# Optimization experiments

Measured on AMD Instinct MI355X. Metric: run time of the kernel, lower is better.

## Reference

```python
import jax, jax.numpy as jnp
import numpy as np

HID = 2048
NH = 16
HD = HID // NH  # 128
EPS = 1e-6
BASE = 10000.0


def _rmsnorm(x, w):
    xf = x.astype(jnp.float32)
    y = xf * jax.lax.rsqrt(jnp.mean(xf * xf, axis=-1, keepdims=True) + EPS)
    return y.astype(x.dtype) * w


def _rope_cos_sin(seq_len, dtype):
    inv_freq = 1.0 / (BASE ** (jnp.arange(0, HD, 2, dtype=jnp.float32) / HD))
    t = jnp.arange(seq_len, dtype=jnp.float32)
    freqs = jnp.outer(t, inv_freq)          # [S, HD/2]
    emb = jnp.concatenate([freqs, freqs], axis=-1)  # [S, HD]
    return jnp.cos(emb).astype(dtype), jnp.sin(emb).astype(dtype)


def _rotate_half(x):
    x1, x2 = jnp.split(x, 2, axis=-1)
    return jnp.concatenate([-x2, x1], axis=-1)


def setup_inputs() -> dict:
    key = jax.random.key(0)
    ks = jax.random.split(key, 8)
    B, S = 2, 2048
    s = 0.02
    return {
        "hidden_states": jax.random.normal(ks[0], (B, S, HID), jnp.float32),
        "Wq": jax.random.normal(ks[1], (HID, HID), jnp.float32) * s,
        "Wk": jax.random.normal(ks[2], (HID, HID), jnp.float32) * s,
        "Wv": jax.random.normal(ks[3], (HID, HID), jnp.float32) * s,
        "Wo": jax.random.normal(ks[4], (HID, HID), jnp.float32) * s,
        "w1": jax.random.normal(ks[5], (HID, HID), jnp.float32) * s,
        "w2": jax.random.normal(ks[6], (HID, HID), jnp.float32) * s,
        "w3": jax.random.normal(ks[7], (HID, HID), jnp.float32) * s,
        "ln1_w": jnp.ones((HID,), jnp.float32),
        "ln2_w": jnp.ones((HID,), jnp.float32),
    }


def reference(hidden_states, Wq, Wk, Wv, Wo, w1, w2, w3, ln1_w, ln2_w):
    B, S, _ = hidden_states.shape
    residual = hidden_states
    x = _rmsnorm(hidden_states, ln1_w)

    # projections -> [B, NH, S, HD]
    q = (x @ Wq).reshape(B, S, NH, HD).transpose(0, 2, 1, 3)
    k = (x @ Wk).reshape(B, S, NH, HD).transpose(0, 2, 1, 3)
    v = (x @ Wv).reshape(B, S, NH, HD).transpose(0, 2, 1, 3)

    cos, sin = _rope_cos_sin(S, x.dtype)  # [S, HD]
    cos = cos[None, None]  # broadcast over batch and heads
    sin = sin[None, None]
    q = q * cos + _rotate_half(q) * sin
    k = k * cos + _rotate_half(k) * sin

    scores = jnp.einsum("bhqd,bhkd->bhqk", q, k) / np.sqrt(HD).astype(np.float32)
    # no attention_mask (torch default path). fp32 softmax.
    attn = jax.nn.softmax(scores.astype(jnp.float32), axis=-1).astype(q.dtype)
    ctx = jnp.einsum("bhqk,bhkd->bhqd", attn, v)  # [B, NH, S, HD]
    ctx = ctx.transpose(0, 2, 1, 3).reshape(B, S, HID)
    attn_out = ctx @ Wo

    h = residual + attn_out
    residual = h
    y = _rmsnorm(h, ln2_w)
    mlp = (jax.nn.silu(y @ w1) * (y @ w3)) @ w2
    return residual + mlp
```

## Files before the change

### kernel.cpp

```cpp
#include <hip/hip_runtime.h>

#define HIDN 2048
#define NHEAD 16
#define HD 128
#define SEQ 2048
#define BATCH 2
#define NROWS (BATCH*SEQ)

typedef __bf16 bf16_t;
typedef bf16_t bf16x8 __attribute__((ext_vector_type(8)));
typedef float f32x4 __attribute__((ext_vector_type(4)));

#define AS1 __attribute__((address_space(1)))
#define AS3 __attribute__((address_space(3)))

__device__ __forceinline__ unsigned short f2bf(float x) {
  union { bf16_t b; unsigned short u; } cv; cv.b = (bf16_t)x; return cv.u;
}

#define MFMA16(a,b,c) __builtin_amdgcn_mfma_f32_16x16x32_bf16((a),(b),(c),0,0,0)

__device__ __forceinline__ void gload16(const void* g, void* l) {
  __builtin_amdgcn_global_load_lds((const AS1 void*)g, (AS3 void*)l, 16, 0, 0);
}

__global__ __launch_bounds__(256) void transpose_all_kernel(
    const float* __restrict__ Wq, const float* __restrict__ Wk,
    const float* __restrict__ Wv, const float* __restrict__ Wo,
    const float* __restrict__ w1, const float* __restrict__ w3,
    const float* __restrict__ w2, unsigned short* __restrict__ wblk) {
  const int z = blockIdx.z;
  const float* W; unsigned short* dstb; int tmode = 0, half = 0;
  switch (z) {
    case 0: W = Wq; dstb = wblk;                       tmode = 1; break;
    case 1: W = Wk; dstb = wblk + (size_t)2048 * HIDN; tmode = 1; break;
    case 2: W = Wv; dstb = wblk + (size_t)4096 * HIDN; break;
    case 3: W = Wo; dstb = wblk + (size_t)6144 * HIDN; break;
    case 4: W = w1; dstb = wblk + (size_t)8192 * HIDN; tmode = 2; half = 0; break;
    case 5: W = w3; dstb = wblk + (size_t)8192 * HIDN; tmode = 2; half = 1; break;
    default: W = w2; dstb = wblk + (size_t)12288 * HIDN; break;
  }
  __shared__ float t[64][69];
  const int tid = threadIdx.x;
  const int bn = blockIdx.x * 64, bk = blockIdx.y * 64;
  const int lc = (tid & 15) * 4, lrw = tid >> 4;
#pragma unroll
  for (int i = 0; i < 4; ++i) {
    int k = bk + lrw + i * 16;
    float4 v = *(const float4*)(W + (long)k * HIDN + bn + lc);
    t[lrw + i * 16][lc] = v.x; t[lrw + i * 16][lc + 1] = v.y;
    t[lrw + i * 16][lc + 2] = v.z; t[lrw + i * 16][lc + 3] = v.w;
  }
  __syncthreads();
  const int nl = tid >> 2, k0 = (tid & 3) * 16;
  int n = bn + nl;
  int dst;
  if (tmode == 0) dst = n;
  else if (tmode == 1) { int d = n & 127; dst = (n & ~127) | ((d & 63) << 1) | (d >> 6); }
  else dst = (n >> 4) * 32 + half * 16 + (n & 15);
  unsigned short* orow = dstb + (long)dst * HIDN + bk + k0;
#pragma unroll
  for (int j = 0; j < 16; j += 4) {
    ushort4 o;
    o.x = f2bf(t[k0 + j][nl]);     o.y = f2bf(t[k0 + j + 1][nl]);
    o.z = f2bf(t[k0 + j + 2][nl]); o.w = f2bf(t[k0 + j + 3][nl]);
    *(ushort4*)(orow + j) = o;
  }
}

__global__ void rope_table_kernel(float* __restrict__ cosT, float* __restrict__ sinT) {
  int s = blockIdx.x, d = threadIdx.x;
  float invf = powf(10000.0f, (-2.0f * (float)d) / 128.0f);
  float ang = (float)s * invf;
  cosT[s * 64 + d] = cosf(ang);
  sinT[s * 64 + d] = sinf(ang);
}

__global__ __launch_bounds__(256) void rmsnorm_kernel(
    const float* __restrict__ x, const float* __restrict__ w, unsigned short* __restrict__ out) {
  long row = blockIdx.x;
  const float* xr = x + row * HIDN;
  int c0 = threadIdx.x * 4;
  float4 v0 = *(const float4*)(xr + c0);
  float4 v1 = *(const float4*)(xr + 1024 + c0);
  float s = v0.x*v0.x + v0.y*v0.y + v0.z*v0.z + v0.w*v0.w
          + v1.x*v1.x + v1.y*v1.y + v1.z*v1.z + v1.w*v1.w;
#pragma unroll
  for (int off = 1; off < 64; off <<= 1) s += __shfl_xor(s, off);
  __shared__ float red[4];
  if ((threadIdx.x & 63) == 0) red[threadIdx.x >> 6] = s;
  __syncthreads();
  float tot = red[0] + red[1] + red[2] + red[3];
  float r = 1.0f / sqrtf(tot * (1.0f / (float)HIDN) + 1e-6f);
  float4 w0 = *(const float4*)(w + c0);
  float4 w1 = *(const float4*)(w + 1024 + c0);
  ushort4 o0, o1;
  o0.x = f2bf(v0.x * r * w0.x); o0.y = f2bf(v0.y * r * w0.y);
  o0.z = f2bf(v0.z * r * w0.z); o0.w = f2bf(v0.w * r * w0.w);
  o1.x = f2bf(v1.x * r * w1.x); o1.y = f2bf(v1.y * r * w1.y);
  o1.z = f2bf(v1.z * r * w1.z); o1.w = f2bf(v1.w * r * w1.w);
  *(ushort4*)(out + row * HIDN + c0) = o0;
  *(ushort4*)(out + row * HIDN + 1024 + c0) = o1;
}

template <int MODE>
__global__ __launch_bounds__(512, 2) void gemm256_kernel(
    const unsigned short* __restrict__ A, const unsigned short* __restrict__ Bt,
    int nbx,
    void* __restrict__ p0, void* __restrict__ p1, void* __restrict__ p2,
    const float* __restrict__ cosT, const float* __restrict__ sinT) {
  __shared__ unsigned short L[65536];
  const int tid = threadIdx.x;
  const int wave = tid >> 6, lane = tid & 63;
  const int lr = lane & 15, lkg = lane >> 4;
  const int wr = wave >> 2, wc = wave & 3;
  const int nwg = (int)gridDim.x;
  const int bid = (int)blockIdx.x;
  const int wg = (bid & 7) * (nwg >> 3) + (bid >> 3);
  const int bx = wg % nbx, by = wg / nbx;
  const long bm = (long)by * 256, bn = (long)bx * 256;
  const int srow = wave * 8 + (lane >> 3);
  const int sslot = (lane & 7) ^ (lane >> 3);
  const unsigned short* Ag = A + (bm + srow) * HIDN + sslot * 8;
  const unsigned short* Bg = Bt + (bn + srow) * HIDN + sslot * 8;
  f32x4 acc[8][4] = {};

#define STAGE256(kt2)                                                            \
  {                                                                              \
    const long ko = (long)(kt2) * 64;                                            \
    unsigned short* Ld = &L[((kt2) & 1) * 32768];                                \
    _Pragma("unroll")                                                            \
    for (int j = 0; j < 4; ++j) {                                                \
      gload16(Ag + ko + (long)j * 64 * HIDN, &Ld[(j * 64 + wave * 8) * 64]);     \
      gload16(Bg + ko + (long)j * 64 * HIDN, &Ld[16384 + (j * 64 + wave * 8) * 64]); \
    }                                                                            \
  }

  STAGE256(0);
  STAGE256(1);
  asm volatile("s_waitcnt vmcnt(8)" ::: "memory");
  __builtin_amdgcn_sched_barrier(0);
  __builtin_amdgcn_s_barrier();

  for (int kt = 0; kt < 32; ++kt) {
    const int d = kt & 1;
    const char* Lb = (const char*)L + d * 65536;
    bf16x8 bfr[4][2];
#pragma unroll
    for (int n = 0; n < 4; ++n) {
      int row = wc * 64 + n * 16 + lr;
      int x7 = row & 7;
#pragma unroll
      for (int ks = 0; ks < 2; ++ks) {
        int s = ks * 4 + lkg;
        bfr[n][ks] = *(const bf16x8*)(Lb + 32768 + row * 128 + ((s ^ x7) << 4));
      }
    }
#pragma unroll
    for (int q = 0; q < 4; ++q) {
      bf16x8 af[2][2];
#pragma unroll
      for (int mm = 0; mm < 2; ++mm) {
        int row = wr * 128 + (q * 2 + mm) * 16 + lr;
        int x7 = row & 7;
#pragma unroll
        for (int ks = 0; ks < 2; ++ks) {
          int s = ks * 4 + lkg;
          af[mm][ks] = *(const bf16x8*)(Lb + row * 128 + ((s ^ x7) << 4));
        }
      }
      __builtin_amdgcn_s_setprio(1);
#pragma unroll
      for (int mm = 0; mm < 2; ++mm)
#pragma unroll
        for (int n = 0; n < 4; ++n) {
          acc[q * 2 + mm][n] = MFMA16(af[mm][0], bfr[n][0], acc[q * 2 + mm][n]);
          acc[q * 2 + mm][n] = MFMA16(af[mm][1], bfr[n][1], acc[q * 2 + mm][n]);
        }
      __builtin_amdgcn_s_setprio(0);
    }
    if (kt == 31) break;
    asm volatile("s_waitcnt lgkmcnt(0)" ::: "memory");
    __builtin_amdgcn_sched_barrier(0);
    __builtin_amdgcn_s_barrier();
    if (kt < 30) {
      STAGE256(kt + 2);
      asm volatile("s_waitcnt vmcnt(8)" ::: "memory");
    } else {
      asm volatile("s_waitcnt vmcnt(0)" ::: "memory");
    }
    __builtin_amdgcn_sched_barrier(0);
    __builtin_amdgcn_s_barrier();
  }
#undef STAGE256

  const int gc0 = (int)bn + wc * 64;
  if (MODE == 1) {
    unsigned short* bout = (unsigned short*)p0;
#pragma unroll
    for (int m = 0; m < 8; ++m) {
      long r0 = bm + wr * 128 + m * 16 + lkg * 4;
#pragma unroll
      for (int n = 0; n < 4; n += 2) {
        int ggrp = (gc0 + n * 16) >> 5;
        long c = (long)ggrp * 16 + lr;
#pragma unroll
        for (int r = 0; r < 4; ++r) {
          float x = acc[m][n][r], g = acc[m][n + 1][r];
          float sv = x / (1.0f + __expf(-x)) * g;
          bout[(r0 + r) * 2048 + c] = f2bf(sv);
        }
      }
    }
  } else {
    int bufid = gc0 >> 11;
    if (bufid == 2) {
      unsigned short* vT = (unsigned short*)p2;
#pragma unroll
      for (int m = 0; m < 8; ++m) {
        long r0 = bm + wr * 128 + m * 16 + lkg * 4;
        long bq = r0 >> 11;
        int s = (int)(r0 & 2047);
#pragma unroll
        for (int n = 0; n < 4; ++n) {
          int wcol = (gc0 + n * 16 + lr) & 2047;
          int hh = wcol >> 7, dd = wcol & 127;
          ushort4 pw;
          pw.x = f2bf(acc[m][n][0]); pw.y = f2bf(acc[m][n][1]);
          pw.z = f2bf(acc[m][n][2]); pw.w = f2bf(acc[m][n][3]);
          *(ushort4*)(vT + ((bq * 16 + hh) * 128 + dd) * (long)SEQ + s) = pw;
        }
      }
    } else {
      unsigned short* dst = (bufid == 0) ? (unsigned short*)p0 : (unsigned short*)p1;
      const float qscale = (bufid == 0) ? 0.08838834764831845f : 1.0f;
#pragma unroll
      for (int m = 0; m < 8; ++m) {
        long r0 = bm + wr * 128 + m * 16 + lkg * 4;
#pragma unroll
        for (int n = 0; n < 4; ++n) {
          int wcol = (gc0 + n * 16 + lr) & 2047;
          int f = wcol & 127, hh = wcol >> 7;
          int j = f >> 1, odd = f & 1;
          int oc = hh * 128 + (odd ? 64 : 0) + j;
#pragma unroll
          for (int r = 0; r < 4; ++r) {
            long row = r0 + r;
            int s = (int)(row & (SEQ - 1));
            float cv = cosT[s * 64 + j], sn = sinT[s * 64 + j];
            float v = acc[m][n][r];
            float o = __shfl_xor(v, 1);
            float res = (odd ? (v * cv + o * sn) : (v * cv - o * sn)) * qscale;
            dst[row * 2048 + oc] = f2bf(res);
          }
        }
      }
    }
  }
}

template <int MODE>
__global__ __launch_bounds__(256) void gemm_kernel(
    const unsigned short* __restrict__ A, const unsigned short* __restrict__ Bt, int N,
    void* __restrict__ p0, const void* __restrict__ p1) {
  __shared__ unsigned short As[128 * 32];
  __shared__ unsigned short Bs[128 * 32];
  const int tid = threadIdx.x;
  const int lane = tid & 63, wave = tid >> 6;
  const int wm = (wave >> 1) * 64, wn = (wave & 1) * 64;
  const int lr = lane & 15, lkg = lane >> 4;
  const long bm = (long)blockIdx.y * 128, bn = (long)blockIdx.x * 128;
  f32x4 acc[4][4] = {};
  const int rA0 = wave * 32 + (lane >> 2);
  const int gs0 = (lane & 3) ^ ((rA0 >> 1) & 3);
  const int gs1 = (lane & 3) ^ (((rA0 + 16) >> 1) & 3);
  const unsigned short* Ag0 = A + (bm + rA0) * HIDN + gs0 * 8;
  const unsigned short* Ag1 = A + (bm + rA0 + 16) * HIDN + gs1 * 8;
  const unsigned short* Bg0 = Bt + (bn + rA0) * HIDN + gs0 * 8;
  const unsigned short* Bg1 = Bt + (bn + rA0 + 16) * HIDN + gs1 * 8;
  unsigned short* lA0 = &As[(wave * 32) * 32];
  unsigned short* lA1 = &As[(wave * 32 + 16) * 32];
  unsigned short* lB0 = &Bs[(wave * 32) * 32];
  unsigned short* lB1 = &Bs[(wave * 32 + 16) * 32];
  for (int k0 = 0; k0 < HIDN; k0 += 32) {
    __syncthreads();
    gload16(Ag0 + k0, lA0);
    gload16(Ag1 + k0, lA1);
    gload16(Bg0 + k0, lB0);
    gload16(Bg1 + k0, lB1);
    __syncthreads();
    bf16x8 af[4], bfr[4];
#pragma unroll
    for (int m = 0; m < 4; ++m) {
      int row = wm + m * 16 + lr;
      af[m] = *(const bf16x8*)((const char*)As + row * 64 + ((lkg ^ ((row >> 1) & 3)) << 4));
    }
#pragma unroll
    for (int n = 0; n < 4; ++n) {
      int row = wn + n * 16 + lr;
      bfr[n] = *(const bf16x8*)((const char*)Bs + row * 64 + ((lkg ^ ((row >> 1) & 3)) << 4));
    }
#pragma unroll
    for (int m = 0; m < 4; ++m)
#pragma unroll
      for (int n = 0; n < 4; ++n) acc[m][n] = MFMA16(af[m], bfr[n], acc[m][n]);
  }
  float* fout = (float*)p0;
  const float* addsrc = (const float*)p1;
#pragma unroll
  for (int m = 0; m < 4; ++m)
#pragma unroll
    for (int n = 0; n < 4; ++n) {
      long r0 = bm + wm + m * 16 + lkg * 4;
      long c = bn + wn + n * 16 + lr;
#pragma unroll
      for (int r = 0; r < 4; ++r) {
        long idx = (r0 + r) * 2048 + c;
        if (MODE == 2) fout[idx] = addsrc[idx] + acc[m][n][r];
        else fout[idx] = fout[idx] + acc[m][n][r];
      }
    }
}

__global__ __launch_bounds__(256) void flash_attn_kernel(
    const unsigned short* __restrict__ Q, const unsigned short* __restrict__ Kb,
    const unsigned short* __restrict__ vT, unsigned short* __restrict__ O) {
  __shared__ unsigned short Ks[2][64 * 128];
  __shared__ unsigned short Vs[2][128 * 64];
  __shared__ unsigned short Ps[4][16][72];
  const int qt = blockIdx.x, h = blockIdx.y, b = blockIdx.z;
  const int tid = threadIdx.x, wave = tid >> 6, lane = tid & 63;
  const int lr = lane & 15, lkg = lane >> 4, lk = lkg * 8;
  const long rowbase = (long)b * SEQ;
  const int qrow0 = qt * 64 + wave * 16;
  bf16x8 aq[4];
#pragma unroll
  for (int ks = 0; ks < 4; ++ks)
    aq[ks] = *(const bf16x8*)(Q + (rowbase + qrow0 + lr) * HIDN + h * HD + ks * 32 + lk);
  const unsigned short* vbase = vT + ((long)(b * 16 + h) * 128) * SEQ;
  const int krl = lane >> 4;
  const int vrl = lane >> 3, vch = lane & 7;
  f32x4 acc[8] = {};
  float m_ = -3.0e38f, l_ = 0.f;

#define STAGEKV(t_, kv0_)                                                          \
  {                                                                                \
    _Pragma("unroll")                                                              \
    for (int j = 0; j < 4; ++j) {                                                  \
      int rl = wave * 16 + j * 4 + krl;                                            \
      int slot = (lane & 15) ^ (rl & 15);                                          \
      gload16(Kb + (rowbase + (kv0_) + rl) * HIDN + h * HD + slot * 8,             \
              &Ks[(t_) & 1][(wave * 16 + j * 4) * 128]);                           \
    }                                                                              \
    _Pragma("unroll")                                                              \
    for (int j = 0; j < 4; ++j) {                                                  \
      int dd = wave * 32 + j * 8 + vrl;                                            \
      int slot = vch ^ (dd & 7);                                                   \
      gload16(vbase + (long)dd * SEQ + (kv0_) + slot * 8,                          \
              &Vs[(t_) & 1][(wave * 32 + j * 8) * 64]);                            \
    }                                                                              \
  }

  STAGEKV(0, 0);

  for (int t = 0; t < SEQ / 64; ++t) {
    asm volatile("s_waitcnt vmcnt(0)" ::: "memory");
    asm volatile("s_barrier" ::: "memory");
    if (t + 1 < SEQ / 64) STAGEKV(t + 1, (long)(t + 1) * 64);
    const char* ksb = (const char*)Ks[t & 1];
    f32x4 sa[4] = {};
#pragma unroll
    for (int n = 0; n < 4; ++n) {
      int row = n * 16 + lr;
#pragma unroll
      for (int ks = 0; ks < 4; ++ks) {
        bf16x8 bk = *(const bf16x8*)(ksb + row * 256 + (((ks * 4 + lkg) ^ (row & 15)) << 4));
        sa[n] = MFMA16(bk, aq[ks], sa[n]);
      }
    }
    float pmax = sa[0][0];
#pragma unroll
    for (int n = 0; n < 4; ++n)
#pragma unroll
      for (int r = 0; r < 4; ++r) pmax = fmaxf(pmax, sa[n][r]);
    pmax = fmaxf(pmax, __shfl_xor(pmax, 16));
    pmax = fmaxf(pmax, __shfl_xor(pmax, 32));
    if (__all(pmax - m_ <= 8.0f)) {
      float psum = 0.f;
#pragma unroll
      for (int n = 0; n < 4; ++n)
#pragma unroll
        for (int r = 0; r < 4; ++r) {
          float p = __expf(sa[n][r] - m_);
          sa[n][r] = p;
          psum += p;
        }
      psum += __shfl_xor(psum, 16);
      psum += __shfl_xor(psum, 32);
      l_ += psum;
    } else {
      float mnew = fmaxf(m_, pmax);
      float corr = __expf(m_ - mnew);
      float psum = 0.f;
#pragma unroll
      for (int n = 0; n < 4; ++n)
#pragma unroll
        for (int r = 0; r < 4; ++r) {
          float p = __expf(sa[n][r] - mnew);
          sa[n][r] = p;
          psum += p;
        }
      psum += __shfl_xor(psum, 16);
      psum += __shfl_xor(psum, 32);
      l_ = l_ * corr + psum;
      m_ = mnew;
      float corr4[4];
#pragma unroll
      for (int r = 0; r < 4; ++r) corr4[r] = __shfl(corr, 4 * lkg + r);
#pragma unroll
      for (int df = 0; df < 8; ++df)
#pragma unroll
        for (int r = 0; r < 4; ++r) acc[df][r] *= corr4[r];
    }
#pragma unroll
    for (int n = 0; n < 4; ++n) {
      ushort4 pw;
      pw.x = f2bf(sa[n][0]); pw.y = f2bf(sa[n][1]);
      pw.z = f2bf(sa[n][2]); pw.w = f2bf(sa[n][3]);
      *(ushort4*)&Ps[wave][lr][n * 16 + 4 * lkg] = pw;
    }
    bf16x8 pa0 = *(const bf16x8*)&Ps[wave][lr][lk];
    bf16x8 pa1 = *(const bf16x8*)&Ps[wave][lr][32 + lk];
    const char* vsb = (const char*)Vs[t & 1];
#pragma unroll
    for (int df = 0; df < 8; ++df) {
      int row = df * 16 + lr;
      int x7 = row & 7;
      bf16x8 bv0 = *(const bf16x8*)(vsb + row * 128 + ((lkg ^ x7) << 4));
      bf16x8 bv1 = *(const bf16x8*)(vsb + row * 128 + (((4 + lkg) ^ x7) << 4));
      acc[df] = MFMA16(pa0, bv0, acc[df]);
      acc[df] = MFMA16(pa1, bv1, acc[df]);
    }
    asm volatile("s_barrier" ::: "memory");
  }
#undef STAGEKV
  float invl = 1.0f / l_;
  float invl4[4];
#pragma unroll
  for (int r = 0; r < 4; ++r) invl4[r] = __shfl(invl, 4 * lkg + r);
#pragma unroll
  for (int r = 0; r < 4; ++r) {
    long orow = rowbase + qrow0 + lkg * 4 + r;
#pragma unroll
    for (int df = 0; df < 8; ++df)
      O[orow * HIDN + h * HD + df * 16 + lr] = f2bf(acc[df][r] * invl4[r]);
  }
}

extern "C" void kernel_launch(void* const* d_in, const int* in_sizes, int n_in,
                              void* d_out, int out_size, void* d_ws, size_t ws_size,
                              hipStream_t stream) {
  const float* hidden = (const float*)d_in[0];
  const float* Wq = (const float*)d_in[1];
  const float* Wk = (const float*)d_in[2];
  const float* Wv = (const float*)d_in[3];
  const float* Wo = (const float*)d_in[4];
  const float* w1 = (const float*)d_in[5];
  const float* w2 = (const float*)d_in[6];
  const float* w3 = (const float*)d_in[7];
  const float* ln1 = (const float*)d_in[8];
  const float* ln2 = (const float*)d_in[9];
  float* out = (float*)d_out;

  char* ws = (char*)d_ws;
  size_t off = 0;
  auto alloc = [&](size_t bytes) -> void* {
    void* p = ws + off;
    off += (bytes + 255) & ~(size_t)255;
    return p;
  };
  unsigned short* wblk = (unsigned short*)alloc((size_t)(2048L * 6 + 2048) * HIDN * 2);
  unsigned short* wQ = wblk;
  unsigned short* wG = wblk + (size_t)8192 * HIDN;
  unsigned short* wO = wblk + (size_t)6144 * HIDN;
  unsigned short* wD = wblk + (size_t)12288 * HIDN;
  unsigned short* xb   = (unsigned short*)alloc((size_t)NROWS * HIDN * 2);
  unsigned short* qb   = (unsigned short*)alloc((size_t)NROWS * HIDN * 2);
  unsigned short* kb   = (unsigned short*)alloc((size_t)NROWS * HIDN * 2);
  unsigned short* vTb  = (unsigned short*)alloc((size_t)NROWS * HIDN * 2);
  unsigned short* ctxb = (unsigned short*)alloc((size_t)NROWS * HIDN * 2);
  float* cosT = (float*)alloc((size_t)SEQ * 64 * 4);
  float* sinT = (float*)alloc((size_t)SEQ * 64 * 4);
  if (off > ws_size) return;

  transpose_all_kernel<<<dim3(HIDN / 64, HIDN / 64, 7), 256, 0, stream>>>(
      Wq, Wk, Wv, Wo, w1, w3, w2, wblk);
  rope_table_kernel<<<SEQ, 64, 0, stream>>>(cosT, sinT);

  rmsnorm_kernel<<<NROWS, 256, 0, stream>>>(hidden, ln1, xb);

  gemm256_kernel<0><<<(6144 / 256) * (NROWS / 256), 512, 0, stream>>>(
      xb, wQ, 6144 / 256, qb, kb, vTb, cosT, sinT);

  flash_attn_kernel<<<dim3(SEQ / 64, NHEAD, BATCH), 256, 0, stream>>>(qb, kb, vTb, ctxb);

  gemm_kernel<2><<<dim3(2048 / 128, NROWS / 128), 256, 0, stream>>>(
      ctxb, wO, 2048, out, hidden);

  rmsnorm_kernel<<<NROWS, 256, 0, stream>>>(out, ln2, xb);

  gemm256_kernel<1><<<(4096 / 256) * (NROWS / 256), 512, 0, stream>>>(
      xb, wG, 4096 / 256, qb, nullptr, nullptr, nullptr, nullptr);

  gemm_kernel<3><<<dim3(2048 / 128, NROWS / 128), 256, 0, stream>>>(
      qb, wD, 2048, out, nullptr);
}
```

Before: 477.1 us.

## Interleave half-tile global-to-LDS loads with MFMA phases in 256x256 GEMM

Restructures the main GEMM k-loop into an 8-phase ping-pong schedule. Global-to-LDS loads are issued as 128-row halves of A and B spread between the MFMA quarters, and barriers sit between the LDS reads and compute phases. The goal is to hide memory latency and LDS traffic behind matrix-core work, similar to hand-scheduled HipKittens-style kernels. The trade is many more barriers and hand-tuned waitcnt counts, which are fragile and could stall if they are wrong.

```diff
diff --git a/kernel.cpp b/kernel.cpp
--- a/kernel.cpp
+++ b/kernel.cpp
@@ -114,85 +114,100 @@
   const int wave = tid >> 6, lane = tid & 63;
   const int lr = lane & 15, lkg = lane >> 4;
   const int wr = wave >> 2, wc = wave & 3;
+  const int x7 = lr & 7;
   const int nwg = (int)gridDim.x;
   const int bid = (int)blockIdx.x;
   const int wg = (bid & 7) * (nwg >> 3) + (bid >> 3);
   const int bx = wg % nbx, by = wg / nbx;
   const long bm = (long)by * 256, bn = (long)bx * 256;
-  const int srow = wave * 8 + (lane >> 3);
   const int sslot = (lane & 7) ^ (lane >> 3);
-  const unsigned short* Ag = A + (bm + srow) * HIDN + sslot * 8;
-  const unsigned short* Bg = Bt + (bn + srow) * HIDN + sslot * 8;
+  const unsigned short* Ag = A + (bm + wave * 8 + (lane >> 3)) * HIDN + sslot * 8;
+  const unsigned short* Bg = Bt + (bn + wave * 8 + (lane >> 3)) * HIDN + sslot * 8;
+  const char* Lc = (const char*)L;
   f32x4 acc[8][4] = {};
-
-#define STAGE256(kt2)                                                            \
-  {                                                                              \
-    const long ko = (long)(kt2) * 64;                                            \
-    unsigned short* Ld = &L[((kt2) & 1) * 32768];                                \
-    _Pragma("unroll")                                                            \
-    for (int j = 0; j < 4; ++j) {                                                \
-      gload16(Ag + ko + (long)j * 64 * HIDN, &Ld[(j * 64 + wave * 8) * 64]);     \
-      gload16(Bg + ko + (long)j * 64 * HIDN, &Ld[16384 + (j * 64 + wave * 8) * 64]); \
-    }                                                                            \
-  }
-
-  STAGE256(0);
-  STAGE256(1);
-  asm volatile("s_waitcnt vmcnt(8)" ::: "memory");
+  bf16x8 af[2][2], bfr[4][2];
+
+#define STG(b, mat, half, tile)                                                   \
+  {                                                                               \
+    const unsigned short* gsrc = ((mat) ? Bg : Ag) + ((long)(half) * 128) * HIDN + (long)(tile) * 64; \
+    unsigned short* ldst = &L[((4 * (b) + 2 * (mat) + (half)) * 8192) + wave * 8 * 64]; \
+    gload16(gsrc, ldst);                                                          \
+    gload16(gsrc + (long)64 * HIDN, ldst + 4096);                                 \
+  }
+#define DSRA(b, q)                                                                \
+  { _Pragma("unroll") for (int mm = 0; mm < 2; ++mm) {                            \
+      int row128 = ((q) * 2 + mm) * 16 + lr;                                      \
+      _Pragma("unroll") for (int ks = 0; ks < 2; ++ks) {                          \
+        int s = ks * 4 + lkg;                                                     \
+        af[mm][ks] = *(const bf16x8*)(Lc + (4 * (b) + wr) * 16384 + row128 * 128 + ((s ^ x7) << 4)); \
+      } } }
+#define DSRB(b)                                                                   \
+  { _Pragma("unroll") for (int n = 0; n < 4; ++n) {                               \
+      int row128 = (wc & 1) * 64 + n * 16 + lr;                                   \
+      _Pragma("unroll") for (int ks = 0; ks < 2; ++ks) {                          \
+        int s = ks * 4 + lkg;                                                     \
+        bfr[n][ks] = *(const bf16x8*)(Lc + (4 * (b) + 2 + (wc >> 1)) * 16384 + row128 * 128 + ((s ^ x7) << 4)); \
+      } } }
+#define MFMAQ(q)                                                                  \
+  { __builtin_amdgcn_s_setprio(1);                                                \
+    _Pragma("unroll") for (int mm = 0; mm < 2; ++mm)                              \
+      _Pragma("unroll") for (int n = 0; n < 4; ++n) {                             \
+        acc[(q) * 2 + mm][n] = MFMA16(af[mm][0], bfr[n][0], acc[(q) * 2 + mm][n]); \
+        acc[(q) * 2 + mm][n] = MFMA16(af[mm][1], bfr[n][1], acc[(q) * 2 + mm][n]); \
+      }                                                                           \
+    __builtin_amdgcn_s_setprio(0); }
+#define BARR __builtin_amdgcn_s_barrier()
+#define LGK0 { asm volatile("s_waitcnt lgkmcnt(0)" ::: "memory"); __builtin_amdgcn_sched_barrier(0); }
+
+  STG(0, 0, 0, 0); STG(0, 0, 1, 0); STG(0, 1, 0, 0); STG(0, 1, 1, 0);
+  STG(1, 1, 0, 1); STG(1, 1, 1, 1); STG(1, 0, 0, 1);
+  asm volatile("s_waitcnt vmcnt(6)" ::: "memory");
   __builtin_amdgcn_sched_barrier(0);
-  __builtin_amdgcn_s_barrier();
-
-  for (int kt = 0; kt < 32; ++kt) {
-    const int d = kt & 1;
-    const char* Lb = (const char*)L + d * 65536;
-    bf16x8 bfr[4][2];
-#pragma unroll
-    for (int n = 0; n < 4; ++n) {
-      int row = wc * 64 + n * 16 + lr;
-      int x7 = row & 7;
-#pragma unroll
-      for (int ks = 0; ks < 2; ++ks) {
-        int s = ks * 4 + lkg;
-        bfr[n][ks] = *(const bf16x8*)(Lb + 32768 + row * 128 + ((s ^ x7) << 4));
-      }
-    }
-#pragma unroll
-    for (int q = 0; q < 4; ++q) {
-      bf16x8 af[2][2];
-#pragma unroll
-      for (int mm = 0; mm < 2; ++mm) {
-        int row = wr * 128 + (q * 2 + mm) * 16 + lr;
-        int x7 = row & 7;
-#pragma unroll
-        for (int ks = 0; ks < 2; ++ks) {
-          int s = ks * 4 + lkg;
-          af[mm][ks] = *(const bf16x8*)(Lb + row * 128 + ((s ^ x7) << 4));
-        }
-      }
-      __builtin_amdgcn_s_setprio(1);
-#pragma unroll
-      for (int mm = 0; mm < 2; ++mm)
-#pragma unroll
-        for (int n = 0; n < 4; ++n) {
-          acc[q * 2 + mm][n] = MFMA16(af[mm][0], bfr[n][0], acc[q * 2 + mm][n]);
-          acc[q * 2 + mm][n] = MFMA16(af[mm][1], bfr[n][1], acc[q * 2 + mm][n]);
-        }
-      __builtin_amdgcn_s_setprio(0);
-    }
-    if (kt == 31) break;
-    asm volatile("s_waitcnt lgkmcnt(0)" ::: "memory");
+  BARR;
+
+  const int NIT = HIDN / 128;
+#pragma unroll 1
+  for (int i = 0; i < NIT; ++i) {
+    const int t2 = 2 * i + 2, t3 = 2 * i + 3;
+    const bool nl_ = (i < NIT - 1);
+    DSRA(0, 0); DSRB(0);
+    STG(1, 0, 1, 2 * i + 1);
+    asm volatile("s_waitcnt lgkmcnt(8)" ::: "memory");
+    BARR; LGK0; MFMAQ(0); BARR;
+    DSRA(0, 1);
+    if (nl_) STG(0, 1, 0, t2);
+    BARR; LGK0; MFMAQ(1); BARR;
+    DSRA(0, 2);
+    if (nl_) STG(0, 1, 1, t2);
+    BARR; LGK0; MFMAQ(2); BARR;
+    DSRA(0, 3);
+    BARR; LGK0; MFMAQ(3);
+    if (nl_) { asm volatile("s_waitcnt vmcnt(4)" ::: "memory"); }
+    else     { asm volatile("s_waitcnt vmcnt(0)" ::: "memory"); }
     __builtin_amdgcn_sched_barrier(0);
-    __builtin_amdgcn_s_barrier();
-    if (kt < 30) {
-      STAGE256(kt + 2);
-      asm volatile("s_waitcnt vmcnt(8)" ::: "memory");
-    } else {
-      asm volatile("s_waitcnt vmcnt(0)" ::: "memory");
-    }
-    __builtin_amdgcn_sched_barrier(0);
-    __builtin_amdgcn_s_barrier();
-  }
-#undef STAGE256
+    BARR;
+    DSRA(1, 0); DSRB(1);
+    if (nl_) STG(0, 0, 0, t2);
+    asm volatile("s_waitcnt lgkmcnt(8)" ::: "memory");
+    BARR; LGK0; MFMAQ(0); BARR;
+    DSRA(1, 1);
+    if (nl_) { STG(0, 0, 1, t2); STG(1, 1, 0, t3); }
+    BARR; LGK0; MFMAQ(1); BARR;
+    DSRA(1, 2);
+    if (nl_) STG(1, 1, 1, t3);
+    BARR; LGK0; MFMAQ(2); BARR;
+    DSRA(1, 3);
+    if (nl_) STG(1, 0, 0, t3);
+    BARR; LGK0; MFMAQ(3);
+    if (nl_) { asm volatile("s_waitcnt vmcnt(6)" ::: "memory"); __builtin_amdgcn_sched_barrier(0); }
+    BARR;
+  }
+#undef STG
+#undef DSRA
+#undef DSRB
+#undef MFMAQ
+#undef BARR
+#undef LGK0
 
   const int gc0 = (int)bn + wc * 64;
   if (MODE == 1) {
```

Result: faster. 463.7 us (-2.8%).
